# Performance work log

Hardware: AMD Instinct MI355X
Metric: run time of the kernel (lower is better)

## Reference

```python
import jax, jax.numpy as jnp
import numpy as np

VP, B, C, H, W = 8, 2, 512, 16, 16
N_HEAD = 8


def setup_inputs() -> dict:
    key = jax.random.key(0)
    k0, k1, k2, k3, k4 = jax.random.split(key, 5)
    x = jax.random.normal(k0, (VP, B, C, H, W), dtype=jnp.float32)
    s = 1.0 / np.sqrt(C)
    Wqkv = jax.random.normal(k1, (C, 3 * C), dtype=jnp.float32) * s
    bqkv = jnp.zeros((3 * C,), dtype=jnp.float32)
    Wo = jax.random.normal(k2, (C, C), dtype=jnp.float32) * s
    bo = jnp.zeros((C,), dtype=jnp.float32)
    return {"x": x, "Wqkv": Wqkv, "bqkv": bqkv, "Wo": Wo, "bo": bo}


def reference(x, Wqkv, bqkv, Wo, bo):
    vp, b, c, h, w = x.shape
    hw = h * w
    T = vp * hw
    hd = c // N_HEAD
    # 'v b c h w -> b (v h w) c'
    xs = jnp.transpose(x, (1, 0, 3, 4, 2)).reshape(b, T, c)
    qkv = xs @ Wqkv + bqkv  # [b, T, 3c]
    q, k, v = jnp.split(qkv, 3, axis=-1)
    def heads(t):
        return jnp.transpose(t.reshape(b, T, N_HEAD, hd), (0, 2, 1, 3))  # [b, nh, T, hd]
    q, k, v = heads(q), heads(k), heads(v)
    scale = 1.0 / np.sqrt(hd)
    att = jnp.einsum('bhqd,bhkd->bhqk', q, k) * scale  # [b, nh, T, T]
    # block-causal mask: token in block i attends to all tokens in blocks 0..i
    blk = jnp.arange(T) // hw
    allowed = blk[None, :] <= blk[:, None]  # [T, T]
    att = jnp.where(allowed, att, -jnp.inf)
    att = jax.nn.softmax(att, axis=-1)
    y = jnp.einsum('bhqk,bhkd->bhqd', att, v)  # [b, nh, T, hd]
    y = jnp.transpose(y, (0, 2, 1, 3)).reshape(b, T, c)
    y = y @ Wo + bo
    # 'b (v h w) c -> v b c h w'
    y = jnp.transpose(y.reshape(b, vp, h, w, c), (1, 0, 4, 2, 3))
    return y
```

## Files before the change

### kernel.cpp

```cpp
#include <hip/hip_runtime.h>
#include <hip/hip_bf16.h>
#include <stdint.h>

#define VPn 8
#define BBn 2
#define CCn 512
#define NHn 8
#define HDn 64
#define Tn  2048
#define Mn  4096
#define N1n 1536
#define Kn  512
#define QSC 0.180336880111120425f

typedef __attribute__((ext_vector_type(8))) short bf16x8;
typedef __attribute__((ext_vector_type(4))) short s16x4;
typedef __attribute__((ext_vector_type(4))) float f32x4;
typedef __attribute__((ext_vector_type(16))) float f32x16;
typedef __attribute__((ext_vector_type(2))) unsigned int u32x2;
typedef unsigned short u16;
typedef unsigned int   u32;

__device__ __forceinline__ u16 f2bf(float f) {
  return __builtin_bit_cast(u16, __float2bfloat16(f));
}
__device__ __forceinline__ u32 cvtpk(float lo, float hi) {
  u32 r;
  asm("v_cvt_pk_bf16_f32 %0, %1, %2" : "=v"(r) : "v"(lo), "v"(hi));
  return r;
}
__device__ __forceinline__ void gload16(const void* g, void* l) {
  __builtin_amdgcn_global_load_lds(
      (const __attribute__((address_space(1))) u32*)g,
      (__attribute__((address_space(3))) u32*)l, 16, 0, 0);
}

__global__ __launch_bounds__(256) void conv_x(const float* __restrict__ x, u16* __restrict__ A) {
  int bi = blockIdx.x;
  int vb = bi >> 5;
  int ct = (bi >> 2) & 7;
  int ht = bi & 3;
  int v = vb >> 1, b = vb & 1;
  __shared__ float t[64][65];
  int tid = threadIdx.x, col = tid & 63, r4 = tid >> 6;
  const float* src = x + ((size_t)vb * CCn + ct * 64) * 256 + ht * 64;
#pragma unroll
  for (int i = 0; i < 16; ++i) {
    int row = i * 4 + r4;
    t[row][col] = src[row * 256 + col];
  }
  __syncthreads();
  u16* dst = A + ((size_t)(b * Tn + v * 256 + ht * 64)) * Kn + ct * 64;
#pragma unroll
  for (int i = 0; i < 16; ++i) {
    int row = i * 4 + r4;
    dst[row * Kn + col] = f2bf(t[col][row]);
  }
}

__global__ __launch_bounds__(256) void convw(const float* __restrict__ Win, u16* __restrict__ Wt,
                                             int R, int Cc) {
  int tpr = Cc >> 6;
  int rt = blockIdx.x / tpr, ct = blockIdx.x % tpr;
  __shared__ float t[64][65];
  int tid = threadIdx.x, col = tid & 63, r4 = tid >> 6;
  const float* src = Win + (size_t)(rt * 64) * Cc + ct * 64;
#pragma unroll
  for (int i = 0; i < 16; ++i) {
    int row = i * 4 + r4;
    t[row][col] = src[row * Cc + col];
  }
  __syncthreads();
  u16* dst = Wt + (size_t)(ct * 64) * R + rt * 64;
#pragma unroll
  for (int i = 0; i < 16; ++i) {
    int row = i * 4 + r4;
    dst[row * R + col] = f2bf(t[col][row]);
  }
}


__global__ __launch_bounds__(256, 2) void gemm_qkv(
    const u16* __restrict__ A, const u16* __restrict__ Bt, const float* __restrict__ bias,
    u16* __restrict__ Qo, u16* __restrict__ Kp, u16* __restrict__ Vp) {
  const int nt = N1n / 128;
  int m0 = (blockIdx.x / nt) * 64;
  int n0 = (blockIdx.x % nt) * 128;
  __shared__ __align__(16) u16 As[64 * 64];
  __shared__ __align__(16) u16 Bs[128 * 64];
  int tid = threadIdx.x, lane = tid & 63, w = tid >> 6;
  int wr = w & 1, wc = w >> 1;
  int li = lane & 15, g = lane >> 4;
  int rsub = lane >> 3, slot = lane & 7;
  int srcslot = slot ^ rsub;
  f32x4 acc[2][4] = {};
  for (int k0 = 0; k0 < Kn; k0 += 64) {
    __syncthreads();
#pragma unroll
    for (int i = 0; i < 2; ++i) {
      int ci = w * 2 + i;
      int row = ci * 8 + rsub;
      gload16(A + (size_t)(m0 + row) * Kn + k0 + srcslot * 8, (char*)As + ci * 1024);
    }
#pragma unroll
    for (int i = 0; i < 4; ++i) {
      int ci = w * 4 + i;
      int row = ci * 8 + rsub;
      gload16(Bt + (size_t)(n0 + row) * Kn + k0 + srcslot * 8, (char*)Bs + ci * 1024);
    }
    __syncthreads();
#pragma unroll
    for (int kk = 0; kk < 2; ++kk) {
      bf16x8 af[2], bfr[4];
#pragma unroll
      for (int mi = 0; mi < 2; ++mi) {
        int row = wr * 32 + mi * 16 + li;
        int sw = ((kk * 4 + g) ^ (row & 7)) * 8;
        af[mi] = *(const bf16x8*)(As + row * 64 + sw);
      }
#pragma unroll
      for (int ni = 0; ni < 4; ++ni) {
        int row = wc * 64 + ni * 16 + li;
        int sw = ((kk * 4 + g) ^ (row & 7)) * 8;
        bfr[ni] = *(const bf16x8*)(Bs + row * 64 + sw);
      }
#pragma unroll
      for (int mi = 0; mi < 2; ++mi)
#pragma unroll
        for (int ni = 0; ni < 4; ++ni)
          acc[mi][ni] = __builtin_amdgcn_mfma_f32_16x16x32_bf16(af[mi], bfr[ni], acc[mi][ni], 0, 0, 0);
    }
  }
#pragma unroll
  for (int ni = 0; ni < 4; ++ni) {
    int n = n0 + wc * 64 + ni * 16 + li;
    float bn = bias[n];
    int sel = n >> 9, c = n & 511, hh = c >> 6, d = c & 63;
    if (sel == 0) {
#pragma unroll
      for (int mi = 0; mi < 2; ++mi) {
#pragma unroll
        for (int r = 0; r < 4; ++r) {
          int m = m0 + wr * 32 + mi * 16 + g * 4 + r;
          int bq = m >> 11, t = m & 2047;
          Qo[((size_t)((bq * NHn + hh) * Tn + t)) * HDn + d] = f2bf((acc[mi][ni][r] + bn) * QSC);
        }
      }
    } else if (sel == 1) {
      int kc = d >> 4, khi = (d >> 3) & 1, kj = d & 7;
#pragma unroll
      for (int mi = 0; mi < 2; ++mi) {
#pragma unroll
        for (int r = 0; r < 4; ++r) {
          int m = m0 + wr * 32 + mi * 16 + g * 4 + r;
          int bq = m >> 11, t = m & 2047;
          size_t off = (size_t)(bq * NHn + hh) * 131072 + (size_t)(t >> 5) * 2048 +
                       kc * 512 + khi * 256 + (t & 31) * 8 + kj;
          Kp[off] = f2bf(acc[mi][ni][r] + bn);
        }
      }
    } else {
      int dh = d >> 5, lqd = d & 31;
#pragma unroll
      for (int mi = 0; mi < 2; ++mi) {
        int mb = m0 + wr * 32 + mi * 16 + g * 4;
        int bq = mb >> 11, t0 = mb & 2047;
        size_t off = (size_t)(bq * NHn + hh) * 131072 + (size_t)(t0 >> 5) * 2048 +
                     dh * 1024 + ((t0 >> 4) & 1) * 512 + lqd * 16 +
                     ((t0 >> 2) & 1) * 8 + ((t0 >> 3) & 1) * 4;
        u32x2 ov;
        ov.x = cvtpk(acc[mi][ni][0] + bn, acc[mi][ni][1] + bn);
        ov.y = cvtpk(acc[mi][ni][2] + bn, acc[mi][ni][3] + bn);
        *(u32x2*)(Vp + off) = ov;
      }
    }
  }
}

__global__ __launch_bounds__(256, 4) void attn(
    const u16* __restrict__ Q, const u16* __restrict__ Kp, const u16* __restrict__ Vp,
    u16* __restrict__ Y) {
  int idx = blockIdx.x;
  int bh = (idx & 7) | (((idx >> 3) & 1) << 3);
  int qt = 63 - (idx >> 4);
  int b = bh >> 3, h = bh & 7;
  int qrow0 = qt << 5;
  int nkeys = ((qt >> 3) + 1) << 8;
  int qtr = nkeys >> 2;
  int tid = threadIdx.x;
  int w = tid >> 6;
  int kbeg = w * qtr, kend = kbeg + qtr;
  int lane = tid & 63;
  int lq = lane & 31;
  int hi = lane >> 5;

  const u16* Qb = Q + ((size_t)(bh * Tn + qrow0)) * HDn;
  const u16* Kb = Kp + (size_t)bh * 131072;
  const u16* Vb = Vp + (size_t)bh * 131072;
  int kof = hi * 256 + lq * 8;
  int vof = lq * 16 + hi * 8;

  bf16x8 qf[4];
  {
    const u16* qp = Qb + (size_t)lq * HDn + hi * 8;
#pragma unroll
    for (int c = 0; c < 4; ++c) qf[c] = *(const bf16x8*)(qp + c * 16);
  }

  float mrun = -1e30f, lrun = 0.f;
  f32x16 oacc0 = {}, oacc1 = {};

  bf16x8 kc[4];
#pragma unroll
  for (int c = 0; c < 4; ++c)
    kc[c] = *(const bf16x8*)(Kb + (size_t)(kbeg >> 5) * 2048 + c * 512 + kof);

  for (int k0 = kbeg; k0 < kend; k0 += 32) {
    int kt = k0 >> 5;
    int ktn = (k0 + 32 < kend) ? (kt + 1) : kt;
    bf16x8 knf[4];
#pragma unroll
    for (int c = 0; c < 4; ++c)
      knf[c] = *(const bf16x8*)(Kb + (size_t)ktn * 2048 + c * 512 + kof);
    const u16* vt = Vb + (size_t)kt * 2048 + vof;
    bf16x8 va0 = *(const bf16x8*)(vt);
    bf16x8 vb0 = *(const bf16x8*)(vt + 512);
    bf16x8 va1 = *(const bf16x8*)(vt + 1024);
    bf16x8 vb1 = *(const bf16x8*)(vt + 1536);

    f32x16 s = {};
    __builtin_amdgcn_s_setprio(1);
#pragma unroll
    for (int c = 0; c < 4; ++c)
      s = __builtin_amdgcn_mfma_f32_32x32x16_bf16(kc[c], qf[c], s, 0, 0, 0);
    __builtin_amdgcn_s_setprio(0);

    float m0 = fmaxf(fmaxf(fmaxf(fmaxf(s[0], s[1]), fmaxf(s[2], s[3])),
                           fmaxf(fmaxf(s[4], s[5]), fmaxf(s[6], s[7]))),
                     fmaxf(fmaxf(fmaxf(s[8], s[9]), fmaxf(s[10], s[11])),
                           fmaxf(fmaxf(s[12], s[13]), fmaxf(s[14], s[15]))));
    float mall = fmaxf(m0, __shfl_xor(m0, 32));
    if (!__all(mall <= mrun + 8.0f)) {
      float mnew = fmaxf(mrun, mall);
      float fc = exp2f(mrun - mnew);
      mrun = mnew;
      lrun *= fc;
#pragma unroll
      for (int j = 0; j < 16; ++j) { oacc0[j] *= fc; oacc1[j] *= fc; }
    }
    float p[16];
#pragma unroll
    for (int j = 0; j < 16; ++j) p[j] = exp2f(s[j] - mrun);
    lrun += (((p[0] + p[1]) + (p[2] + p[3])) + ((p[4] + p[5]) + (p[6] + p[7]))) +
            (((p[8] + p[9]) + (p[10] + p[11])) + ((p[12] + p[13]) + (p[14] + p[15])));

    bf16x8 pfA, pfB;
    {
      __attribute__((ext_vector_type(4))) int pa = {
          (int)cvtpk(p[0], p[1]), (int)cvtpk(p[2], p[3]),
          (int)cvtpk(p[4], p[5]), (int)cvtpk(p[6], p[7])};
      __attribute__((ext_vector_type(4))) int pb = {
          (int)cvtpk(p[8], p[9]), (int)cvtpk(p[10], p[11]),
          (int)cvtpk(p[12], p[13]), (int)cvtpk(p[14], p[15])};
      pfA = __builtin_bit_cast(bf16x8, pa);
      pfB = __builtin_bit_cast(bf16x8, pb);
    }

    __builtin_amdgcn_s_setprio(1);
    oacc0 = __builtin_amdgcn_mfma_f32_32x32x16_bf16(va0, pfA, oacc0, 0, 0, 0);
    oacc0 = __builtin_amdgcn_mfma_f32_32x32x16_bf16(vb0, pfB, oacc0, 0, 0, 0);
    oacc1 = __builtin_amdgcn_mfma_f32_32x32x16_bf16(va1, pfA, oacc1, 0, 0, 0);
    oacc1 = __builtin_amdgcn_mfma_f32_32x32x16_bf16(vb1, pfB, oacc1, 0, 0, 0);
    __builtin_amdgcn_s_setprio(0);
#pragma unroll
    for (int c = 0; c < 4; ++c) kc[c] = knf[c];
  }

  lrun += __shfl_xor(lrun, 32);

  __shared__ float Ol[4][32][68];
  __shared__ float ml[2][4][32];
  {
    float* op = &Ol[w][lq][hi * 4];
#pragma unroll
    for (int a = 0; a < 4; ++a) {
      f32x4 v0 = {oacc0[4 * a], oacc0[4 * a + 1], oacc0[4 * a + 2], oacc0[4 * a + 3]};
      f32x4 v1 = {oacc1[4 * a], oacc1[4 * a + 1], oacc1[4 * a + 2], oacc1[4 * a + 3]};
      *(f32x4*)(op + a * 8) = v0;
      *(f32x4*)(op + 32 + a * 8) = v1;
    }
    if (lane < 32) { ml[0][w][lq] = mrun; ml[1][w][lq] = lrun; }
  }
  __syncthreads();

#pragma unroll
  for (int task = tid; task < 512; task += 256) {
    int q = task >> 4, quad = task & 15;
    float m0v = ml[0][0][q], m1v = ml[0][1][q], m2v = ml[0][2][q], m3v = ml[0][3][q];
    float mx = fmaxf(fmaxf(m0v, m1v), fmaxf(m2v, m3v));
    float w0 = exp2f(m0v - mx), w1 = exp2f(m1v - mx);
    float w2 = exp2f(m2v - mx), w3 = exp2f(m3v - mx);
    float l = ml[1][0][q] * w0 + ml[1][1][q] * w1 + ml[1][2][q] * w2 + ml[1][3][q] * w3;
    float inv = 1.0f / l;
    f32x4 o0 = *(const f32x4*)&Ol[0][q][quad * 4];
    f32x4 o1 = *(const f32x4*)&Ol[1][q][quad * 4];
    f32x4 o2 = *(const f32x4*)&Ol[2][q][quad * 4];
    f32x4 o3 = *(const f32x4*)&Ol[3][q][quad * 4];
    float y0 = (o0[0] * w0 + o1[0] * w1 + o2[0] * w2 + o3[0] * w3) * inv;
    float y1 = (o0[1] * w0 + o1[1] * w1 + o2[1] * w2 + o3[1] * w3) * inv;
    float y2 = (o0[2] * w0 + o1[2] * w1 + o2[2] * w2 + o3[2] * w3) * inv;
    float y3 = (o0[3] * w0 + o1[3] * w1 + o2[3] * w2 + o3[3] * w3) * inv;
    u32x2 yv;
    yv.x = cvtpk(y0, y1);
    yv.y = cvtpk(y2, y3);
    *(u32x2*)(Y + ((size_t)(b * Tn + qrow0 + q)) * CCn + h * HDn + quad * 4) = yv;
  }
}

__global__ __launch_bounds__(256, 4) void gemm_out(
    const u16* __restrict__ A, const u16* __restrict__ Bt, const float* __restrict__ bias,
    float* __restrict__ out) {
  const int nt = 8;
  int m0 = (blockIdx.x / nt) * 64;
  int n0 = (blockIdx.x % nt) * 64;
  __shared__ __align__(16) u16 As[64 * 64];
  __shared__ __align__(16) u16 Bs[64 * 64];
  int tid = threadIdx.x, lane = tid & 63, w = tid >> 6;
  int wr = w & 1, wc = w >> 1;
  int li = lane & 15, g = lane >> 4;
  int rsub = lane >> 3, slot = lane & 7;
  int srcslot = slot ^ rsub;
  f32x4 acc[2][2] = {};
  for (int k0 = 0; k0 < Kn; k0 += 64) {
    __syncthreads();
#pragma unroll
    for (int i = 0; i < 2; ++i) {
      int ci = w * 2 + i;
      int row = ci * 8 + rsub;
      gload16(A  + (size_t)(m0 + row) * Kn + k0 + srcslot * 8, (char*)As + ci * 1024);
      gload16(Bt + (size_t)(n0 + row) * Kn + k0 + srcslot * 8, (char*)Bs + ci * 1024);
    }
    __syncthreads();
#pragma unroll
    for (int kk = 0; kk < 2; ++kk) {
      bf16x8 af[2], bfr[2];
#pragma unroll
      for (int mi = 0; mi < 2; ++mi) {
        int row = wr * 32 + mi * 16 + li;
        int sw = ((kk * 4 + g) ^ (row & 7)) * 8;
        af[mi] = *(const bf16x8*)(As + row * 64 + sw);
      }
#pragma unroll
      for (int ni = 0; ni < 2; ++ni) {
        int row = wc * 32 + ni * 16 + li;
        int sw = ((kk * 4 + g) ^ (row & 7)) * 8;
        bfr[ni] = *(const bf16x8*)(Bs + row * 64 + sw);
      }
#pragma unroll
      for (int mi = 0; mi < 2; ++mi)
#pragma unroll
        for (int ni = 0; ni < 2; ++ni)
          acc[mi][ni] = __builtin_amdgcn_mfma_f32_16x16x32_bf16(af[mi], bfr[ni], acc[mi][ni], 0, 0, 0);
    }
  }
  int b = m0 >> 11, v = (m0 >> 8) & 7, hw0 = m0 & 255;
  float* ob = out + (size_t)((v * 2 + b) * 512) * 256;
#pragma unroll
  for (int ni = 0; ni < 2; ++ni) {
    int n = n0 + wc * 32 + ni * 16 + li;
    float bn = bias[n];
#pragma unroll
    for (int mi = 0; mi < 2; ++mi) {
      int hw = hw0 + wr * 32 + mi * 16 + g * 4;
      f32x4 y;
#pragma unroll
      for (int r = 0; r < 4; ++r) y[r] = acc[mi][ni][r] + bn;
      *(f32x4*)(ob + (size_t)n * 256 + hw) = y;
    }
  }
}

extern "C" void kernel_launch(void* const* d_in, const int* in_sizes, int n_in,
                              void* d_out, int out_size, void* d_ws, size_t ws_size,
                              hipStream_t stream) {
  (void)in_sizes; (void)n_in; (void)out_size; (void)ws_size;
  const float* x    = (const float*)d_in[0];
  const float* Wqkv = (const float*)d_in[1];
  const float* bqkv = (const float*)d_in[2];
  const float* Wo   = (const float*)d_in[3];
  const float* bo   = (const float*)d_in[4];
  float* out = (float*)d_out;
  char* ws = (char*)d_ws;
  const size_t MB = 1ull << 20;
  u16*   Abf   = (u16*)(ws + 0);
  u16*   WqkvT = (u16*)(ws + 4 * MB);
  u16*   WoT   = (u16*)(ws + 5 * MB + 512 * 1024);
  u16*   Qb    = (u16*)(ws + 6 * MB);
  u16*   Kb    = (u16*)(ws + 10 * MB);
  u16*   VTb   = (u16*)(ws + 14 * MB);

  conv_x<<<512, 256, 0, stream>>>(x, Abf);
  convw<<<192, 256, 0, stream>>>(Wqkv, WqkvT, Kn, N1n);
  convw<<<64, 256, 0, stream>>>(Wo, WoT, Kn, CCn);
  gemm_qkv<<<64 * 12, 256, 0, stream>>>(Abf, WqkvT, bqkv, Qb, Kb, VTb);
  attn<<<1024, 256, 0, stream>>>(Qb, Kb, VTb, Abf);
  gemm_out<<<64 * 8, 256, 0, stream>>>(Abf, WoT, bo, out);
}
```

Before: 62.22 us.

## Double-buffer LDS tiles in QKV and output GEMMs; merge weight conversion launches

Both GEMM kernels now use two LDS buffers per operand. The next K-tile is prefetched with async global-to-LDS loads while MFMAs run on the current tile, and explicit vmcnt waits plus barriers order the two. This is meant to hide global load latency that the single-buffer loop with two syncthreads per step left exposed. The two weight-transpose launches are also merged into one launch to save a kernel launch. In exchange, LDS use doubles, which may limit occupancy, and the QKV launch bound is raised to 3 blocks per CU.

```diff
diff --git a/kernel.cpp b/kernel.cpp
--- a/kernel.cpp
+++ b/kernel.cpp
@@ -58,10 +58,12 @@
   }
 }
 
-__global__ __launch_bounds__(256) void convw(const float* __restrict__ Win, u16* __restrict__ Wt,
-                                             int R, int Cc) {
-  int tpr = Cc >> 6;
-  int rt = blockIdx.x / tpr, ct = blockIdx.x % tpr;
+__global__ __launch_bounds__(256) void convw(const float* __restrict__ Wqkv, const float* __restrict__ Wo,
+                                             u16* __restrict__ WqkvT, u16* __restrict__ WoT) {
+  int bi = blockIdx.x;
+  const float* Win; u16* Wt; int Cc, rt, ct;
+  if (bi < 192) { Win = Wqkv; Wt = WqkvT; Cc = N1n; rt = bi / 24; ct = bi % 24; }
+  else { bi -= 192; Win = Wo; Wt = WoT; Cc = CCn; rt = bi / 8; ct = bi % 8; }
   __shared__ float t[64][65];
   int tid = threadIdx.x, col = tid & 63, r4 = tid >> 6;
   const float* src = Win + (size_t)(rt * 64) * Cc + ct * 64;
@@ -71,44 +73,59 @@
     t[row][col] = src[row * Cc + col];
   }
   __syncthreads();
-  u16* dst = Wt + (size_t)(ct * 64) * R + rt * 64;
+  u16* dst = Wt + (size_t)(ct * 64) * Kn + rt * 64;
 #pragma unroll
   for (int i = 0; i < 16; ++i) {
     int row = i * 4 + r4;
-    dst[row * R + col] = f2bf(t[col][row]);
-  }
-}
-
-
-__global__ __launch_bounds__(256, 2) void gemm_qkv(
+    dst[row * Kn + col] = f2bf(t[col][row]);
+  }
+}
+
+
+__global__ __launch_bounds__(256, 3) void gemm_qkv(
     const u16* __restrict__ A, const u16* __restrict__ Bt, const float* __restrict__ bias,
     u16* __restrict__ Qo, u16* __restrict__ Kp, u16* __restrict__ Vp) {
   const int nt = N1n / 128;
   int m0 = (blockIdx.x / nt) * 64;
   int n0 = (blockIdx.x % nt) * 128;
-  __shared__ __align__(16) u16 As[64 * 64];
-  __shared__ __align__(16) u16 Bs[128 * 64];
+  __shared__ __align__(16) u16 As[2][64 * 64];
+  __shared__ __align__(16) u16 Bs[2][128 * 64];
   int tid = threadIdx.x, lane = tid & 63, w = tid >> 6;
   int wr = w & 1, wc = w >> 1;
   int li = lane & 15, g = lane >> 4;
   int rsub = lane >> 3, slot = lane & 7;
   int srcslot = slot ^ rsub;
   f32x4 acc[2][4] = {};
-  for (int k0 = 0; k0 < Kn; k0 += 64) {
-    __syncthreads();
-#pragma unroll
-    for (int i = 0; i < 2; ++i) {
-      int ci = w * 2 + i;
-      int row = ci * 8 + rsub;
-      gload16(A + (size_t)(m0 + row) * Kn + k0 + srcslot * 8, (char*)As + ci * 1024);
-    }
-#pragma unroll
-    for (int i = 0; i < 4; ++i) {
-      int ci = w * 4 + i;
-      int row = ci * 8 + rsub;
-      gload16(Bt + (size_t)(n0 + row) * Kn + k0 + srcslot * 8, (char*)Bs + ci * 1024);
-    }
-    __syncthreads();
+
+#define QKV_STAGE(buf, kk0)                                                    \
+  {                                                                            \
+    _Pragma("unroll")                                                          \
+    for (int i = 0; i < 2; ++i) {                                              \
+      int ci = w * 2 + i;                                                      \
+      int row = ci * 8 + rsub;                                                 \
+      gload16(A + (size_t)(m0 + row) * Kn + (kk0) + srcslot * 8,               \
+              (char*)&As[buf][0] + ci * 1024);                                 \
+    }                                                                          \
+    _Pragma("unroll")                                                          \
+    for (int i = 0; i < 4; ++i) {                                              \
+      int ci = w * 4 + i;                                                      \
+      int row = ci * 8 + rsub;                                                 \
+      gload16(Bt + (size_t)(n0 + row) * Kn + (kk0) + srcslot * 8,              \
+              (char*)&Bs[buf][0] + ci * 1024);                                 \
+    }                                                                          \
+  }
+
+  QKV_STAGE(0, 0);
+#pragma unroll
+  for (int step = 0; step < 8; ++step) {
+    const int cur = step & 1;
+    if (step < 7) {
+      QKV_STAGE(cur ^ 1, (step + 1) * 64);
+      asm volatile("s_waitcnt vmcnt(6)");
+    } else {
+      asm volatile("s_waitcnt vmcnt(0)");
+    }
+    __builtin_amdgcn_s_barrier();
 #pragma unroll
     for (int kk = 0; kk < 2; ++kk) {
       bf16x8 af[2], bfr[4];
@@ -116,13 +133,13 @@
       for (int mi = 0; mi < 2; ++mi) {
         int row = wr * 32 + mi * 16 + li;
         int sw = ((kk * 4 + g) ^ (row & 7)) * 8;
-        af[mi] = *(const bf16x8*)(As + row * 64 + sw);
+        af[mi] = *(const bf16x8*)(&As[cur][0] + row * 64 + sw);
       }
 #pragma unroll
       for (int ni = 0; ni < 4; ++ni) {
         int row = wc * 64 + ni * 16 + li;
         int sw = ((kk * 4 + g) ^ (row & 7)) * 8;
-        bfr[ni] = *(const bf16x8*)(Bs + row * 64 + sw);
+        bfr[ni] = *(const bf16x8*)(&Bs[cur][0] + row * 64 + sw);
       }
 #pragma unroll
       for (int mi = 0; mi < 2; ++mi)
@@ -130,6 +147,9 @@
         for (int ni = 0; ni < 4; ++ni)
           acc[mi][ni] = __builtin_amdgcn_mfma_f32_16x16x32_bf16(af[mi], bfr[ni], acc[mi][ni], 0, 0, 0);
     }
+    asm volatile("s_waitcnt lgkmcnt(0)");
+    __builtin_amdgcn_sched_barrier(0);
+    __builtin_amdgcn_s_barrier();
   }
 #pragma unroll
   for (int ni = 0; ni < 4; ++ni) {
@@ -323,24 +343,39 @@
   const int nt = 8;
   int m0 = (blockIdx.x / nt) * 64;
   int n0 = (blockIdx.x % nt) * 64;
-  __shared__ __align__(16) u16 As[64 * 64];
-  __shared__ __align__(16) u16 Bs[64 * 64];
+  __shared__ __align__(16) u16 As[2][64 * 64];
+  __shared__ __align__(16) u16 Bs[2][64 * 64];
   int tid = threadIdx.x, lane = tid & 63, w = tid >> 6;
   int wr = w & 1, wc = w >> 1;
   int li = lane & 15, g = lane >> 4;
   int rsub = lane >> 3, slot = lane & 7;
   int srcslot = slot ^ rsub;
   f32x4 acc[2][2] = {};
-  for (int k0 = 0; k0 < Kn; k0 += 64) {
-    __syncthreads();
-#pragma unroll
-    for (int i = 0; i < 2; ++i) {
-      int ci = w * 2 + i;
-      int row = ci * 8 + rsub;
-      gload16(A  + (size_t)(m0 + row) * Kn + k0 + srcslot * 8, (char*)As + ci * 1024);
-      gload16(Bt + (size_t)(n0 + row) * Kn + k0 + srcslot * 8, (char*)Bs + ci * 1024);
-    }
-    __syncthreads();
+
+#define OUT_STAGE(buf, kk0)                                                    \
+  {                                                                            \
+    _Pragma("unroll")                                                          \
+    for (int i = 0; i < 2; ++i) {                                              \
+      int ci = w * 2 + i;                                                      \
+      int row = ci * 8 + rsub;                                                 \
+      gload16(A + (size_t)(m0 + row) * Kn + (kk0) + srcslot * 8,               \
+              (char*)&As[buf][0] + ci * 1024);                                 \
+      gload16(Bt + (size_t)(n0 + row) * Kn + (kk0) + srcslot * 8,              \
+              (char*)&Bs[buf][0] + ci * 1024);                                 \
+    }                                                                          \
+  }
+
+  OUT_STAGE(0, 0);
+#pragma unroll
+  for (int step = 0; step < 8; ++step) {
+    const int cur = step & 1;
+    if (step < 7) {
+      OUT_STAGE(cur ^ 1, (step + 1) * 64);
+      asm volatile("s_waitcnt vmcnt(4)");
+    } else {
+      asm volatile("s_waitcnt vmcnt(0)");
+    }
+    __builtin_amdgcn_s_barrier();
 #pragma unroll
     for (int kk = 0; kk < 2; ++kk) {
       bf16x8 af[2], bfr[2];
@@ -348,13 +383,13 @@
       for (int mi = 0; mi < 2; ++mi) {
         int row = wr * 32 + mi * 16 + li;
         int sw = ((kk * 4 + g) ^ (row & 7)) * 8;
-        af[mi] = *(const bf16x8*)(As + row * 64 + sw);
+        af[mi] = *(const bf16x8*)(&As[cur][0] + row * 64 + sw);
       }
 #pragma unroll
       for (int ni = 0; ni < 2; ++ni) {
         int row = wc * 32 + ni * 16 + li;
         int sw = ((kk * 4 + g) ^ (row & 7)) * 8;
-        bfr[ni] = *(const bf16x8*)(Bs + row * 64 + sw);
+        bfr[ni] = *(const bf16x8*)(&Bs[cur][0] + row * 64 + sw);
       }
 #pragma unroll
       for (int mi = 0; mi < 2; ++mi)
@@ -362,6 +397,9 @@
         for (int ni = 0; ni < 2; ++ni)
           acc[mi][ni] = __builtin_amdgcn_mfma_f32_16x16x32_bf16(af[mi], bfr[ni], acc[mi][ni], 0, 0, 0);
     }
+    asm volatile("s_waitcnt lgkmcnt(0)");
+    __builtin_amdgcn_sched_barrier(0);
+    __builtin_amdgcn_s_barrier();
   }
   int b = m0 >> 11, v = (m0 >> 8) & 7, hw0 = m0 & 255;
   float* ob = out + (size_t)((v * 2 + b) * 512) * 256;
@@ -400,8 +438,7 @@
   u16*   VTb   = (u16*)(ws + 14 * MB);
 
   conv_x<<<512, 256, 0, stream>>>(x, Abf);
-  convw<<<192, 256, 0, stream>>>(Wqkv, WqkvT, Kn, N1n);
-  convw<<<64, 256, 0, stream>>>(Wo, WoT, Kn, CCn);
+  convw<<<256, 256, 0, stream>>>(Wqkv, Wo, WqkvT, WoT);
   gemm_qkv<<<64 * 12, 256, 0, stream>>>(Abf, WqkvT, bqkv, Qb, Kb, VTb);
   attn<<<1024, 256, 0, stream>>>(Qb, Kb, VTb, Abf);
   gemm_out<<<64 * 8, 256, 0, stream>>>(Abf, WoT, bo, out);
```

Result: faster. 60.54 us (-2.7%).
